# Kernel optimization log

Measured on AMD Instinct MI355X. Metric: run time of the kernel, lower is better.

Reference implementation:

```python
import jax, jax.numpy as jnp
import numpy as np

N_NODES = 100000
N_EDGES = 1600000
D_IN = 256
D_OUT = 256


def _init_linear(key, out_f, in_f):
    # torch nn.Linear default: U(-1/sqrt(in_f), 1/sqrt(in_f))
    kw, kb = jax.random.split(key)
    bound = 1.0 / np.sqrt(in_f)
    W = jax.random.uniform(kw, (out_f, in_f), jnp.float32, -bound, bound)
    b = jax.random.uniform(kb, (out_f,), jnp.float32, -bound, bound)
    return W, b


def setup_inputs() -> dict:
    key = jax.random.key(0)
    ks = jax.random.split(key, 7)
    x = jax.random.normal(ks[0], (N_NODES, D_IN), jnp.float32)
    edge_index = jax.random.randint(ks[1], (2, N_EDGES), 0, N_NODES, jnp.int64)
    W1, b1 = _init_linear(ks[2], D_OUT, D_IN)
    W2, b2 = _init_linear(ks[3], D_OUT // 2, D_OUT)
    W3, b3 = _init_linear(ks[4], D_OUT // 2, D_OUT)
    Wd1, bd1 = _init_linear(ks[5], D_OUT, D_OUT)
    Wd2, bd2 = _init_linear(ks[6], 1, D_OUT)
    return {"x": x, "edge_index": edge_index,
            "W1": W1, "b1": b1, "W2": W2, "b2": b2, "W3": W3, "b3": b3,
            "Wd1": Wd1, "bd1": bd1, "Wd2": Wd2, "bd2": bd2}


def _l2norm(x):
    return x / jnp.linalg.norm(x, axis=-1, keepdims=True)


def reference(x, edge_index, W1, b1, W2, b2, W3, b3, Wd1, bd1, Wd2, bd2):
    src, dst = edge_index[0], edge_index[1]  # source_to_target flow
    x = jax.nn.relu(x @ W1.T + b1)           # [N, D_OUT]
    x = _l2norm(x)
    for _ in range(2):
        # sum-aggregate neighbor messages: scatter-add x[src] into dst
        nm = jax.ops.segment_sum(x[src], dst, num_segments=N_NODES)  # [N, D_OUT]
        x = jax.nn.relu(jnp.concatenate([x @ W2.T + b2, nm @ W3.T + b3], axis=-1))
        x = _l2norm(x)
    x = jax.nn.relu(x @ Wd1.T + bd1)
    return x @ Wd2.T + bd2                    # [N, 1]
```

## Files before the change

### kernel.cpp

```cpp
#include <hip/hip_runtime.h>
#include <math.h>


typedef _Float16 f16x8 __attribute__((ext_vector_type(8)));
typedef float    f32x16 __attribute__((ext_vector_type(16)));

constexpr int DIM = 256;
constexpr int BM  = 128;
constexpr int BK  = 32;
constexpr int SA  = 40;
constexpr int SW  = 40;

__device__ __forceinline__ unsigned pk_hi2(float a, float b) {
    unsigned short ha = __builtin_bit_cast(unsigned short, (_Float16)a);
    unsigned short hb = __builtin_bit_cast(unsigned short, (_Float16)b);
    return (unsigned)ha | ((unsigned)hb << 16);
}
__device__ __forceinline__ unsigned pk_lo2(float a, float b) {
    _Float16 ha = (_Float16)a, hb = (_Float16)b;
    unsigned short la = __builtin_bit_cast(unsigned short, (_Float16)(a - (float)ha));
    unsigned short lb = __builtin_bit_cast(unsigned short, (_Float16)(b - (float)hb));
    return (unsigned)la | ((unsigned)lb << 16);
}
__device__ __forceinline__ unsigned pack_pair(float v) {
    _Float16 hi = (_Float16)v;
    _Float16 lo = (_Float16)(v - (float)hi);
    return (unsigned)__builtin_bit_cast(unsigned short, hi)
         | ((unsigned)__builtin_bit_cast(unsigned short, lo) << 16);
}

template <int AMODE, int EPI>
__global__ __launch_bounds__(256, 2)
void gemm_mfma(const void* __restrict__ Av,
               const float* __restrict__ WA, const float* __restrict__ WB,
               const float* __restrict__ bA, const float* __restrict__ bB,
               void* __restrict__ outv,
               const float* __restrict__ wd2, const float* __restrict__ bd2,
               float* __restrict__ out1, int M)
{
    __shared__ __align__(16) _Float16 smem[30720];
    _Float16* As_hi = smem;
    _Float16* As_lo = smem + 5120;
    _Float16* Ws_hi = smem + 10240;
    _Float16* Ws_lo = smem + 20480;

    const int tid  = threadIdx.x;
    const int lane = tid & 63;
    const int w    = tid >> 6;
    const int rh   = w >> 1;
    const int ch   = w & 1;
    const int l31  = lane & 31;
    const int lh   = lane >> 5;
    const int bm0  = blockIdx.x * BM;

    const unsigned* Au = (const unsigned*)Av;
    const int srow = tid >> 3;
    const int sch  = (tid & 7) * 4;

    uint4  pa[4];
    float4 pw[8];

    auto fetchA = [&](int t) {
        const int k0 = t * BK;
        #pragma unroll
        for (int i = 0; i < 4; ++i) {
            const int gr = bm0 + srow + 32 * i;
            uint4 v = {0u, 0u, 0u, 0u};
            if (gr < M) v = *(const uint4*)&Au[(size_t)gr * 256 + k0 + sch];
            pa[i] = v;
        }
    };
    auto fetchW = [&](int t) {
        const int k0 = t * BK;
        #pragma unroll
        for (int i = 0; i < 8; ++i) {
            const int r = srow + 32 * i;
            const float* src = (r < 128) ? &WA[(size_t)r * 256]
                                         : &WB[(size_t)(r - 128) * 256];
            pw[i] = *(const float4*)&src[k0 + sch];
        }
    };
    auto stageA = [&]() {
        #pragma unroll
        for (int i = 0; i < 4; ++i) {
            const int r = srow + 32 * i;
            unsigned h0, h1, l0, l1;
            if (AMODE == 0) {
                const float x0 = __builtin_bit_cast(float, pa[i].x);
                const float x1 = __builtin_bit_cast(float, pa[i].y);
                const float x2 = __builtin_bit_cast(float, pa[i].z);
                const float x3 = __builtin_bit_cast(float, pa[i].w);
                h0 = pk_hi2(x0, x1); h1 = pk_hi2(x2, x3);
                l0 = pk_lo2(x0, x1); l1 = pk_lo2(x2, x3);
            } else {
                h0 = __builtin_amdgcn_perm(pa[i].y, pa[i].x, 0x05040100u);
                l0 = __builtin_amdgcn_perm(pa[i].y, pa[i].x, 0x07060302u);
                h1 = __builtin_amdgcn_perm(pa[i].w, pa[i].z, 0x05040100u);
                l1 = __builtin_amdgcn_perm(pa[i].w, pa[i].z, 0x07060302u);
            }
            uint2 th; th.x = h0; th.y = h1;
            uint2 tl; tl.x = l0; tl.y = l1;
            *(uint2*)&As_hi[r * SA + sch] = th;
            *(uint2*)&As_lo[r * SA + sch] = tl;
        }
    };
    auto stageW = [&]() {
        #pragma unroll
        for (int i = 0; i < 8; ++i) {
            const int r = srow + 32 * i;
            uint2 th; th.x = pk_hi2(pw[i].x, pw[i].y); th.y = pk_hi2(pw[i].z, pw[i].w);
            uint2 tl; tl.x = pk_lo2(pw[i].x, pw[i].y); tl.y = pk_lo2(pw[i].z, pw[i].w);
            *(uint2*)&Ws_hi[r * SW + sch] = th;
            *(uint2*)&Ws_lo[r * SW + sch] = tl;
        }
    };

    f32x16 acc[2][4];
    #pragma unroll
    for (int tr = 0; tr < 2; ++tr)
        #pragma unroll
        for (int tc = 0; tc < 4; ++tc)
            #pragma unroll
            for (int i = 0; i < 16; ++i) acc[tr][tc][i] = 0.0f;

    fetchA(0); fetchW(0);

    #pragma unroll 1
    for (int t = 0; t < DIM / BK; ++t) {
        stageA(); stageW();
        __syncthreads();
        if (t < DIM / BK - 1) { fetchA(t + 1); fetchW(t + 1); }

        #pragma unroll
        for (int ks = 0; ks < 2; ++ks) {
            f16x8 ah[2], al[2], wh[4], wl[4];
            #pragma unroll
            for (int tr = 0; tr < 2; ++tr) {
                const int off = (rh * 64 + tr * 32 + l31) * SA + ks * 16 + lh * 8;
                ah[tr] = *(const f16x8*)&As_hi[off];
                al[tr] = *(const f16x8*)&As_lo[off];
            }
            #pragma unroll
            for (int tc = 0; tc < 4; ++tc) {
                const int off = (ch * 128 + tc * 32 + l31) * SW + ks * 16 + lh * 8;
                wh[tc] = *(const f16x8*)&Ws_hi[off];
                wl[tc] = *(const f16x8*)&Ws_lo[off];
            }
            #pragma unroll
            for (int tr = 0; tr < 2; ++tr)
                #pragma unroll
                for (int tc = 0; tc < 4; ++tc) {
                    acc[tr][tc] = __builtin_amdgcn_mfma_f32_32x32x16_f16(ah[tr], wh[tc], acc[tr][tc], 0, 0, 0);
                    acc[tr][tc] = __builtin_amdgcn_mfma_f32_32x32x16_f16(ah[tr], wl[tc], acc[tr][tc], 0, 0, 0);
                    acc[tr][tc] = __builtin_amdgcn_mfma_f32_32x32x16_f16(al[tr], wh[tc], acc[tr][tc], 0, 0, 0);
                }
        }
        __syncthreads();
    }


    if (EPI == 0) {
        float* z = (float*)outv;
        #pragma unroll
        for (int tr = 0; tr < 2; ++tr)
            #pragma unroll
            for (int i = 0; i < 16; ++i) {
                const int r  = rh * 64 + tr * 32 + 4 * lh + (i & 3) + 8 * (i >> 2);
                const int gr = bm0 + r;
                if (gr < M) {
                    #pragma unroll
                    for (int tc = 0; tc < 4; ++tc)
                        z[(size_t)gr * 256 + ch * 128 + tc * 32 + l31] = acc[tr][tc][i];
                }
            }
        return;
    }

    {
        float bias[4];
        #pragma unroll
        for (int tc = 0; tc < 4; ++tc)
            bias[tc] = (ch ? bB : bA)[tc * 32 + l31];
        #pragma unroll
        for (int tr = 0; tr < 2; ++tr)
            #pragma unroll
            for (int tc = 0; tc < 4; ++tc)
                #pragma unroll
                for (int i = 0; i < 16; ++i)
                    acc[tr][tc][i] = fmaxf(acc[tr][tc][i] + bias[tc], 0.0f);
    }

    float* red = (float*)smem;

    if (EPI == 1) {
        float ss[2][16];
        #pragma unroll
        for (int tr = 0; tr < 2; ++tr)
            #pragma unroll
            for (int i = 0; i < 16; ++i) {
                float s = 0.f;
                #pragma unroll
                for (int tc = 0; tc < 4; ++tc) s += acc[tr][tc][i] * acc[tr][tc][i];
                #pragma unroll
                for (int m = 1; m < 32; m <<= 1) s += __shfl_xor(s, m);
                ss[tr][i] = s;
            }
        const int j  = l31;
        const int ji = j & 15, jt = j >> 4;
        red[ch * 128 + rh * 64 + jt * 32 + 4 * lh + (ji & 3) + 8 * (ji >> 2)] = ss[jt][ji];
        __syncthreads();

        unsigned* hp = (unsigned*)outv;
        #pragma unroll
        for (int tr = 0; tr < 2; ++tr)
            #pragma unroll
            for (int i = 0; i < 16; ++i) {
                const int rl = rh * 64 + tr * 32 + 4 * lh + (i & 3) + 8 * (i >> 2);
                const float inv = 1.0f / sqrtf(red[rl] + red[128 + rl]);
                const int gr = bm0 + rl;
                if (gr < M) {
                    #pragma unroll
                    for (int tc = 0; tc < 4; ++tc)
                        hp[(size_t)gr * 256 + ch * 128 + tc * 32 + l31] =
                            pack_pair(acc[tr][tc][i] * inv);
                }
            }
        return;
    }

    {
        float wv[4];
        #pragma unroll
        for (int tc = 0; tc < 4; ++tc) wv[tc] = wd2[ch * 128 + tc * 32 + l31];
        float dd[2][16];
        #pragma unroll
        for (int tr = 0; tr < 2; ++tr)
            #pragma unroll
            for (int i = 0; i < 16; ++i) {
                float s = 0.f;
                #pragma unroll
                for (int tc = 0; tc < 4; ++tc) s += acc[tr][tc][i] * wv[tc];
                #pragma unroll
                for (int m = 1; m < 32; m <<= 1) s += __shfl_xor(s, m);
                dd[tr][i] = s;
            }
        const int j  = l31;
        const int ji = j & 15, jt = j >> 4;
        red[ch * 128 + rh * 64 + jt * 32 + 4 * lh + (ji & 3) + 8 * (ji >> 2)] = dd[jt][ji];
        __syncthreads();
        if (tid < 128) {
            const int gr = bm0 + tid;
            if (gr < M) out1[gr] = red[tid] + red[128 + tid] + bd2[0];
        }
    }
}


__global__ void hist_kernel(const int* __restrict__ ei, int E, int* __restrict__ cnt)
{
    int e = blockIdx.x * blockDim.x + threadIdx.x;
    if (e < E) atomicAdd(&cnt[ei[E + e]], 1);
}

__global__ void scan1_kernel(const int* __restrict__ cnt, int n,
                             int* __restrict__ rp, int* __restrict__ sums)
{
    __shared__ int sm[1024];
    const int tid = threadIdx.x;
    const int i = blockIdx.x * 1024 + tid;
    const int v = (i < n) ? cnt[i] : 0;
    sm[tid] = v;
    __syncthreads();
    for (int off = 1; off < 1024; off <<= 1) {
        int t = (tid >= off) ? sm[tid - off] : 0;
        __syncthreads();
        sm[tid] += t;
        __syncthreads();
    }
    if (i < n) rp[i] = sm[tid] - v;
    if (tid == 1023) sums[blockIdx.x] = sm[tid];
}

__global__ void scan2_kernel(int* __restrict__ sums, int n)
{
    __shared__ int sm[128];
    const int tid = threadIdx.x;
    const int v = (tid < n) ? sums[tid] : 0;
    sm[tid] = v;
    __syncthreads();
    for (int off = 1; off < 128; off <<= 1) {
        int t = (tid >= off) ? sm[tid - off] : 0;
        __syncthreads();
        sm[tid] += t;
        __syncthreads();
    }
    if (tid < n) sums[tid] = sm[tid] - v;
}

__global__ void scan3_kernel(int* __restrict__ rp, const int* __restrict__ sums,
                             int* __restrict__ cursor, int n, int E)
{
    int i = blockIdx.x * blockDim.x + threadIdx.x;
    if (i < n) {
        int v = rp[i] + sums[i >> 10];
        rp[i] = v;
        cursor[i] = v;
    }
    if (i == 0) rp[n] = E;
}

__global__ void fill_kernel(const int* __restrict__ ei, int E,
                            int* __restrict__ cursor, int* __restrict__ esrc)
{
    int e = blockIdx.x * blockDim.x + threadIdx.x;
    if (e < E) {
        int d = ei[E + e];
        int p = atomicAdd(&cursor[d], 1);
        esrc[p] = ei[e];
    }
}

__global__ void fin_kernel(const float* __restrict__ z, const int* __restrict__ rp,
                           const int* __restrict__ esrc,
                           const float* __restrict__ b2, const float* __restrict__ b3,
                           unsigned* __restrict__ hp, int M)
{
    const int gid  = blockIdx.x * blockDim.x + threadIdx.x;
    const int v    = gid >> 6;
    const int lane = gid & 63;
    if (v >= M) return;
    const int beg = rp[v], end = rp[v + 1];

    float2 a0 = {0.f, 0.f}, a1 = {0.f, 0.f};
    int j = beg;
    for (; j + 1 < end; j += 2) {
        const int s0 = esrc[j], s1 = esrc[j + 1];
        const float2 g0 = *(const float2*)&z[(size_t)s0 * DIM + 128 + lane * 2];
        const float2 g1 = *(const float2*)&z[(size_t)s1 * DIM + 128 + lane * 2];
        a0.x += g0.x; a0.y += g0.y;
        a1.x += g1.x; a1.y += g1.y;
    }
    if (j < end) {
        const int s0 = esrc[j];
        const float2 g0 = *(const float2*)&z[(size_t)s0 * DIM + 128 + lane * 2];
        a0.x += g0.x; a0.y += g0.y;
    }
    a0.x += a1.x; a0.y += a1.y;

    const float2 z1 = *(const float2*)&z[(size_t)v * DIM + lane * 2];
    const float2 v2 = *(const float2*)&b2[lane * 2];
    const float2 v3 = *(const float2*)&b3[lane * 2];
    float u1x = fmaxf(z1.x + v2.x, 0.f), u1y = fmaxf(z1.y + v2.y, 0.f);
    float u2x = fmaxf(a0.x + v3.x, 0.f), u2y = fmaxf(a0.y + v3.y, 0.f);

    float ss = u1x * u1x + u1y * u1y + u2x * u2x + u2y * u2y;
    #pragma unroll
    for (int off = 32; off > 0; off >>= 1) ss += __shfl_xor(ss, off);
    const float inv = 1.0f / sqrtf(ss);

    uint2 p1; p1.x = pack_pair(u1x * inv); p1.y = pack_pair(u1y * inv);
    uint2 p2; p2.x = pack_pair(u2x * inv); p2.y = pack_pair(u2y * inv);
    *(uint2*)&hp[(size_t)v * DIM + lane * 2]       = p1;
    *(uint2*)&hp[(size_t)v * DIM + 128 + lane * 2] = p2;
}


extern "C" void kernel_launch(void* const* d_in, const int* in_sizes, int n_in,
                              void* d_out, int out_size, void* d_ws, size_t ws_size,
                              hipStream_t stream)
{
    const float* x   = (const float*)d_in[0];
    const int*   ei  = (const int*)d_in[1];
    const float* W1  = (const float*)d_in[2];
    const float* b1  = (const float*)d_in[3];
    const float* W2  = (const float*)d_in[4];
    const float* b2  = (const float*)d_in[5];
    const float* W3  = (const float*)d_in[6];
    const float* b3  = (const float*)d_in[7];
    const float* Wd1 = (const float*)d_in[8];
    const float* bd1 = (const float*)d_in[9];
    const float* Wd2 = (const float*)d_in[10];
    const float* bd2 = (const float*)d_in[11];
    float* out = (float*)d_out;

    const int M = in_sizes[0] / DIM;
    const int E = in_sizes[1] / 2;

    unsigned* hp  = (unsigned*)d_ws;
    float*    z   = (float*)(hp + (size_t)M * DIM);
    int*   rp     = (int*)(z + (size_t)M * DIM);
    int*   cursor = rp + (M + 1);
    int*   esrc   = cursor + M;
    int*   sums   = esrc + E;

    hipMemsetAsync(cursor, 0, sizeof(int) * M, stream);

    const int gb  = (M + BM - 1) / BM;
    const int eb  = (E + 255) / 256;
    const int nb1 = (M + 1023) / 1024;
    const int wb  = (M * 64 + 255) / 256;

    hist_kernel<<<eb, 256, 0, stream>>>(ei, E, cursor);
    scan1_kernel<<<nb1, 1024, 0, stream>>>(cursor, M, rp, sums);
    scan2_kernel<<<1, 128, 0, stream>>>(sums, nb1);
    scan3_kernel<<<(M + 255) / 256, 256, 0, stream>>>(rp, sums, cursor, M, E);
    fill_kernel<<<eb, 256, 0, stream>>>(ei, E, cursor, esrc);

    gemm_mfma<0, 1><<<gb, 256, 0, stream>>>(
        x, W1, W1 + 128 * DIM, b1, b1 + 128, hp, nullptr, nullptr, nullptr, M);

    for (int it = 0; it < 2; ++it) {
        gemm_mfma<1, 0><<<gb, 256, 0, stream>>>(
            hp, W2, W3, nullptr, nullptr, z, nullptr, nullptr, nullptr, M);
        fin_kernel<<<wb, 256, 0, stream>>>(z, rp, esrc, b2, b3, hp, M);
    }

    gemm_mfma<1, 2><<<gb, 256, 0, stream>>>(
        hp, Wd1, Wd1 + 128 * DIM, bd1, bd1 + 128, nullptr, Wd2, bd2, out, M);
}
```

Before: 872.4 us.

## Co-launch CSR build with GEMMs and stage neighbor indices via readlane

The histogram kernel is merged into the first GEMM launch as extra blocks, and the CSR fill kernel is merged into the first W2/W3 GEMM launch, so the edge work overlaps with dense compute and two launches disappear. Each edge block now handles four edges per thread. The aggregation kernel loads up to 64 neighbor indices per wave in one coalesced read, broadcasts them with readlane, and keeps four independent accumulators so more gathers are in flight. In exchange, atomic-heavy blocks compete with GEMM blocks for CUs, and the 4-way accumulation changes float summation order.

```diff
diff --git a/kernel.cpp b/kernel.cpp
--- a/kernel.cpp
+++ b/kernel.cpp
@@ -30,8 +30,8 @@
 }
 
 template <int AMODE, int EPI>
-__global__ __launch_bounds__(256, 2)
-void gemm_mfma(const void* __restrict__ Av,
+__device__ __forceinline__
+void gemm_body(const void* __restrict__ Av,
                const float* __restrict__ WA, const float* __restrict__ WB,
                const float* __restrict__ bA, const float* __restrict__ bB,
                void* __restrict__ outv,
@@ -255,12 +255,59 @@
     }
 }
 
-
-__global__ void hist_kernel(const int* __restrict__ ei, int E, int* __restrict__ cnt)
-{
-    int e = blockIdx.x * blockDim.x + threadIdx.x;
-    if (e < E) atomicAdd(&cnt[ei[E + e]], 1);
-}
+__global__ __launch_bounds__(256, 2)
+void gemm_l1(const void* __restrict__ Av,
+             const float* __restrict__ WA, const float* __restrict__ WB,
+             const float* __restrict__ bA, const float* __restrict__ bB,
+             void* __restrict__ outv, int M, int gb,
+             const int* __restrict__ ei, int E, int* __restrict__ cnt)
+{
+    if ((int)blockIdx.x < gb) {
+        gemm_body<0, 1>(Av, WA, WB, bA, bB, outv, nullptr, nullptr, nullptr, M);
+    } else {
+        const int base = ((int)blockIdx.x - gb) * 1024 + threadIdx.x;
+        #pragma unroll
+        for (int k = 0; k < 4; ++k) {
+            const int e = base + k * 256;
+            if (e < E) atomicAdd(&cnt[ei[E + e]], 1);
+        }
+    }
+}
+
+template <int DO_FILL>
+__global__ __launch_bounds__(256, 2)
+void gemm_z(const void* __restrict__ Av,
+            const float* __restrict__ WA, const float* __restrict__ WB,
+            void* __restrict__ outv, int M, int gb,
+            const int* __restrict__ ei, int E,
+            int* __restrict__ cursor, int* __restrict__ esrc)
+{
+    if ((int)blockIdx.x < gb) {
+        gemm_body<1, 0>(Av, WA, WB, nullptr, nullptr, outv, nullptr, nullptr, nullptr, M);
+    } else if (DO_FILL) {
+        const int base = ((int)blockIdx.x - gb) * 1024 + threadIdx.x;
+        #pragma unroll
+        for (int k = 0; k < 4; ++k) {
+            const int e = base + k * 256;
+            if (e < E) {
+                int d = ei[E + e];
+                int p = atomicAdd(&cursor[d], 1);
+                esrc[p] = ei[e];
+            }
+        }
+    }
+}
+
+__global__ __launch_bounds__(256, 2)
+void gemm_head(const void* __restrict__ Av,
+               const float* __restrict__ WA, const float* __restrict__ WB,
+               const float* __restrict__ bA, const float* __restrict__ bB,
+               const float* __restrict__ wd2, const float* __restrict__ bd2,
+               float* __restrict__ out1, int M)
+{
+    gemm_body<1, 2>(Av, WA, WB, bA, bB, nullptr, wd2, bd2, out1, M);
+}
+
 
 __global__ void scan1_kernel(const int* __restrict__ cnt, int n,
                              int* __restrict__ rp, int* __restrict__ sums)
@@ -309,49 +356,56 @@
     if (i == 0) rp[n] = E;
 }
 
-__global__ void fill_kernel(const int* __restrict__ ei, int E,
-                            int* __restrict__ cursor, int* __restrict__ esrc)
-{
-    int e = blockIdx.x * blockDim.x + threadIdx.x;
-    if (e < E) {
-        int d = ei[E + e];
-        int p = atomicAdd(&cursor[d], 1);
-        esrc[p] = ei[e];
-    }
-}
-
-__global__ void fin_kernel(const float* __restrict__ z, const int* __restrict__ rp,
-                           const int* __restrict__ esrc,
-                           const float* __restrict__ b2, const float* __restrict__ b3,
-                           unsigned* __restrict__ hp, int M)
-{
-    const int gid  = blockIdx.x * blockDim.x + threadIdx.x;
-    const int v    = gid >> 6;
-    const int lane = gid & 63;
+__global__ __launch_bounds__(256)
+void fin_kernel(const float* __restrict__ z, const int* __restrict__ rp,
+                const int* __restrict__ esrc,
+                const float* __restrict__ b2, const float* __restrict__ b3,
+                unsigned* __restrict__ hp, int M)
+{
+    const int v    = blockIdx.x * 4 + (threadIdx.x >> 6);
+    const int lane = threadIdx.x & 63;
     if (v >= M) return;
     const int beg = rp[v], end = rp[v + 1];
-
-    float2 a0 = {0.f, 0.f}, a1 = {0.f, 0.f};
-    int j = beg;
-    for (; j + 1 < end; j += 2) {
-        const int s0 = esrc[j], s1 = esrc[j + 1];
-        const float2 g0 = *(const float2*)&z[(size_t)s0 * DIM + 128 + lane * 2];
-        const float2 g1 = *(const float2*)&z[(size_t)s1 * DIM + 128 + lane * 2];
-        a0.x += g0.x; a0.y += g0.y;
-        a1.x += g1.x; a1.y += g1.y;
-    }
-    if (j < end) {
-        const int s0 = esrc[j];
-        const float2 g0 = *(const float2*)&z[(size_t)s0 * DIM + 128 + lane * 2];
-        a0.x += g0.x; a0.y += g0.y;
-    }
-    a0.x += a1.x; a0.y += a1.y;
+    const int deg = end - beg;
 
     const float2 z1 = *(const float2*)&z[(size_t)v * DIM + lane * 2];
-    const float2 v2 = *(const float2*)&b2[lane * 2];
-    const float2 v3 = *(const float2*)&b3[lane * 2];
-    float u1x = fmaxf(z1.x + v2.x, 0.f), u1y = fmaxf(z1.y + v2.y, 0.f);
-    float u2x = fmaxf(a0.x + v3.x, 0.f), u2y = fmaxf(a0.y + v3.y, 0.f);
+    const float2 c2 = *(const float2*)&b2[lane * 2];
+    const float2 c3 = *(const float2*)&b3[lane * 2];
+
+    const float* z2 = z + 128;
+    float ax0 = 0.f, ay0 = 0.f, ax1 = 0.f, ay1 = 0.f;
+    float ax2 = 0.f, ay2 = 0.f, ax3 = 0.f, ay3 = 0.f;
+
+    for (int base = 0; base < deg; base += 64) {
+        const int cnt = min(64, deg - base);
+        int myidx = 0;
+        if (lane < cnt) myidx = esrc[beg + base + lane];
+        int j = 0;
+        for (; j + 3 < cnt; j += 4) {
+            const int s0 = __builtin_amdgcn_readlane(myidx, j);
+            const int s1 = __builtin_amdgcn_readlane(myidx, j + 1);
+            const int s2 = __builtin_amdgcn_readlane(myidx, j + 2);
+            const int s3 = __builtin_amdgcn_readlane(myidx, j + 3);
+            const float2 g0 = *(const float2*)&z2[(size_t)s0 * DIM + lane * 2];
+            const float2 g1 = *(const float2*)&z2[(size_t)s1 * DIM + lane * 2];
+            const float2 g2 = *(const float2*)&z2[(size_t)s2 * DIM + lane * 2];
+            const float2 g3 = *(const float2*)&z2[(size_t)s3 * DIM + lane * 2];
+            ax0 += g0.x; ay0 += g0.y;
+            ax1 += g1.x; ay1 += g1.y;
+            ax2 += g2.x; ay2 += g2.y;
+            ax3 += g3.x; ay3 += g3.y;
+        }
+        for (; j < cnt; ++j) {
+            const int s0 = __builtin_amdgcn_readlane(myidx, j);
+            const float2 g0 = *(const float2*)&z2[(size_t)s0 * DIM + lane * 2];
+            ax0 += g0.x; ay0 += g0.y;
+        }
+    }
+    const float sx = (ax0 + ax1) + (ax2 + ax3);
+    const float sy = (ay0 + ay1) + (ay2 + ay3);
+
+    const float u1x = fmaxf(z1.x + c2.x, 0.f), u1y = fmaxf(z1.y + c2.y, 0.f);
+    const float u2x = fmaxf(sx + c3.x, 0.f),  u2y = fmaxf(sy + c3.y, 0.f);
 
     float ss = u1x * u1x + u1y * u1y + u2x * u2x + u2y * u2y;
     #pragma unroll
@@ -396,25 +450,23 @@
     hipMemsetAsync(cursor, 0, sizeof(int) * M, stream);
 
     const int gb  = (M + BM - 1) / BM;
-    const int eb  = (E + 255) / 256;
+    const int hb  = (E + 1023) / 1024;
     const int nb1 = (M + 1023) / 1024;
-    const int wb  = (M * 64 + 255) / 256;
-
-    hist_kernel<<<eb, 256, 0, stream>>>(ei, E, cursor);
+    const int fb  = (M + 3) / 4;
+
+    gemm_l1<<<gb + hb, 256, 0, stream>>>(
+        x, W1, W1 + 128 * DIM, b1, b1 + 128, hp, M, gb, ei, E, cursor);
+
     scan1_kernel<<<nb1, 1024, 0, stream>>>(cursor, M, rp, sums);
     scan2_kernel<<<1, 128, 0, stream>>>(sums, nb1);
     scan3_kernel<<<(M + 255) / 256, 256, 0, stream>>>(rp, sums, cursor, M, E);
-    fill_kernel<<<eb, 256, 0, stream>>>(ei, E, cursor, esrc);
-
-    gemm_mfma<0, 1><<<gb, 256, 0, stream>>>(
-        x, W1, W1 + 128 * DIM, b1, b1 + 128, hp, nullptr, nullptr, nullptr, M);
-
-    for (int it = 0; it < 2; ++it) {
-        gemm_mfma<1, 0><<<gb, 256, 0, stream>>>(
-            hp, W2, W3, nullptr, nullptr, z, nullptr, nullptr, nullptr, M);
-        fin_kernel<<<wb, 256, 0, stream>>>(z, rp, esrc, b2, b3, hp, M);
-    }
-
-    gemm_mfma<1, 2><<<gb, 256, 0, stream>>>(
-        hp, Wd1, Wd1 + 128 * DIM, bd1, bd1 + 128, nullptr, Wd2, bd2, out, M);
-}
+
+    gemm_z<1><<<gb + hb, 256, 0, stream>>>(hp, W2, W3, z, M, gb, ei, E, cursor, esrc);
+    fin_kernel<<<fb, 256, 0, stream>>>(z, rp, esrc, b2, b3, hp, M);
+
+    gemm_z<0><<<gb, 256, 0, stream>>>(hp, W2, W3, z, M, gb, nullptr, 0, nullptr, nullptr);
+    fin_kernel<<<fb, 256, 0, stream>>>(z, rp, esrc, b2, b3, hp, M);
+
+    gemm_head<<<gb, 256, 0, stream>>>(
+        hp, Wd1, Wd1 + 128 * DIM, bd1, bd1 + 128, Wd2, bd2, out, M);
+}
```

New measurement: 733.9 us. -15.9%, faster.
